# Performance work log

Measured on AMD Instinct MI355X. Metric: run time of the kernel, lower is better.

Reference implementation:

```python
import jax, jax.numpy as jnp
import numpy as np

N, M, A, F = 100000, 12, 64, 41  # atoms, neighbors, atom_fea_len, nbr_fea_len
EPS = 1e-5


def setup_inputs() -> dict:
    key = jax.random.key(0)
    ks = jax.random.split(key, 8)
    return {
        "atom_fea": jax.random.normal(ks[0], (N, A), jnp.float32),
        "nbr_fea": jax.random.normal(ks[1], (N, M, F), jnp.float32),
        "nbr_fea_idx": jax.random.randint(ks[2], (N, M), 0, N),
        "W_full": jax.random.normal(ks[3], (3, 2 * A + F, 2 * A), jnp.float32) / np.sqrt(2 * A + F).astype(np.float32),
        "b_full": jnp.zeros((3, 2 * A), jnp.float32),
        "g1": jnp.ones((3, 2 * A), jnp.float32),
        "bt1": jnp.zeros((3, 2 * A), jnp.float32),
        "g2": jnp.ones((3, A), jnp.float32),
        "bt2": jnp.zeros((3, A), jnp.float32),
        "W_scale": jax.random.normal(ks[4], (2, F, F), jnp.float32) / np.sqrt(F).astype(np.float32),
        "b_scale": jnp.zeros((2, F), jnp.float32),
        "W_fuse": jax.random.normal(ks[5], (3 * A, A), jnp.float32) / np.sqrt(3 * A).astype(np.float32),
        "b_fuse": jnp.zeros((A,), jnp.float32),
    }


def _bn(x, g, b):
    # training-mode BatchNorm1d over flattened leading dims (per-feature stats)
    x2 = x.reshape(-1, x.shape[-1])
    mu = x2.mean(0)
    var = x2.var(0)
    xn = (x2 - mu) * jax.lax.rsqrt(var + EPS)
    return (xn * g + b).reshape(x.shape)


def _conv_layer(atom_fea, nbr_fea, idx, W, b, g1, bt1, g2, bt2):
    # standard CGCNN ConvLayer
    nbr_atom = atom_fea[idx]                                   # [N,M,A] gather
    self_fea = jnp.broadcast_to(atom_fea[:, None, :], nbr_atom.shape)
    total = jnp.concatenate([self_fea, nbr_atom, nbr_fea], -1)  # [N,M,2A+F]
    z = _bn(total @ W + b, g1, bt1)                            # [N,M,2A]
    filt, core = jnp.split(z, 2, axis=-1)
    summed = (jax.nn.sigmoid(filt) * jax.nn.softplus(core)).sum(1)  # [N,A]
    summed = _bn(summed, g2, bt2)
    return jax.nn.softplus(atom_fea + summed)


def reference(atom_fea, nbr_fea, nbr_fea_idx, W_full, b_full, g1, bt1, g2, bt2,
              W_scale, b_scale, W_fuse, b_fuse):
    outs = []
    for i in range(3):  # scales [1, 2, 3]
        nf = nbr_fea if i == 0 else nbr_fea @ W_scale[i - 1] + b_scale[i - 1]
        outs.append(_conv_layer(atom_fea, nf, nbr_fea_idx,
                                W_full[i], b_full[i], g1[i], bt1[i], g2[i], bt2[i]))
    cat = jnp.concatenate(outs, -1)            # [N, 3A]
    return jax.nn.relu(cat @ W_fuse + b_fuse)  # [N, A]
```

## Files before the change

kernel.cpp:

```cpp
#include <hip/hip_runtime.h>
#include <math.h>

#define NATOMS 100000
#define M 12
#define A 64
#define F 41
#define C1 128
#define TOTF 169
#define NMROWS (NATOMS * M)

#define OFF_WEFF   0
#define OFF_BEFF   15744
#define OFF_SUM1   16128
#define OFF_SQ1    16512
#define OFF_SUM2   16896
#define OFF_SQ2    17088
#define OFF_SCA    17280
#define OFF_SHA    17664
#define OFF_SCB    18048
#define OFF_SHB    18240
#define OFF_P      32768
#define OFF_SUMMED (OFF_P + (size_t)NATOMS*768)
#define OFF_Q      OFF_P

__device__ __forceinline__ float sigmoidf_(float x) {
    return 1.0f / (1.0f + __expf(-x));
}
__device__ __forceinline__ float softplusf_(float x) {
    return fmaxf(x, 0.0f) + __logf(1.0f + __expf(-fabsf(x)));
}

__global__ void k_weff(const float* __restrict__ Wf, const float* __restrict__ bf,
                       const float* __restrict__ Wsc, const float* __restrict__ bsc,
                       float* __restrict__ ws) {
    int j = threadIdx.x;
    float* We = ws + OFF_WEFF;
    float* be = ws + OFF_BEFF;
    for (int s = 0; s < 3; ++s) {
        float bb = bf[s * C1 + j];
        if (s > 0) {
            for (int q = 0; q < F; ++q)
                bb += bsc[(s - 1) * F + q] * Wf[(s * TOTF + 128 + q) * C1 + j];
        }
        be[s * C1 + j] = bb;
        for (int k = 0; k < F; ++k) {
            float v;
            if (s == 0) {
                v = Wf[(0 * TOTF + 128 + k) * C1 + j];
            } else {
                v = 0.0f;
                for (int q = 0; q < F; ++q)
                    v += Wsc[((s - 1) * F + k) * F + q] * Wf[(s * TOTF + 128 + q) * C1 + j];
            }
            We[(s * F + k) * C1 + j] = v;
        }
    }
}

__global__ __launch_bounds__(256) void k_pall(const float* __restrict__ atom,
                                              const float* __restrict__ Wf,
                                              float* __restrict__ ws) {
    int u = threadIdx.x;
    int s = blockIdx.x;
    float wcol[A];
    int colw = u & 127;
#pragma unroll
    for (int k = 0; k < A; ++k) {
        int row = (u < 128) ? k : (A + k);
        wcol[k] = Wf[(s * TOTF + row) * C1 + colw];
    }
    float* P = ws + OFF_P;
    for (int a = blockIdx.y; a < NATOMS; a += gridDim.y) {
        const float* ar = atom + (size_t)a * A;
        float acc = 0.0f;
#pragma unroll
        for (int k = 0; k < A; ++k) acc = fmaf(ar[k], wcol[k], acc);
        P[(size_t)a * 768 + s * 256 + u] = acc;
    }
}

template <int PASS>
__global__ __launch_bounds__(192) void k_conv(const float* __restrict__ nbr,
                                              const int* __restrict__ idx,
                                              float* __restrict__ ws) {
    int tid = threadIdx.x;
    int s = tid >> 6;
    int j = tid & 63;
    const float* We = ws + OFF_WEFF;
    const float* be = ws + OFF_BEFF;
    const float* P = ws + OFF_P;
    float w1[F], w2[F];
#pragma unroll
    for (int k = 0; k < F; ++k) {
        w1[k] = We[(s * F + k) * C1 + j];
        w2[k] = We[(s * F + k) * C1 + 64 + j];
    }
    float b1 = be[s * C1 + j], b2 = be[s * C1 + 64 + j];
    float sc1 = 0.f, sh1 = 0.f, sc2 = 0.f, sh2 = 0.f;
    if (PASS == 1) {
        sc1 = ws[OFF_SCA + s * C1 + j];
        sh1 = ws[OFF_SHA + s * C1 + j];
        sc2 = ws[OFF_SCA + s * C1 + 64 + j];
        sh2 = ws[OFF_SHA + s * C1 + 64 + j];
    }
    float accA = 0.f, accB = 0.f, accC = 0.f, accD = 0.f;
    float* summed = ws + OFF_SUMMED;
    for (int a = blockIdx.x; a < NATOMS; a += gridDim.x) {
        float ps1 = P[(size_t)a * 768 + s * 256 + j];
        float ps2 = P[(size_t)a * 768 + s * 256 + 64 + j];
        float hsum = 0.0f;
        for (int m = 0; m < M; ++m) {
            int pair = a * M + m;
            int row = idx[pair];
            const float* x = nbr + (size_t)pair * F;
            float z1 = b1 + ps1 + P[(size_t)row * 768 + s * 256 + 128 + j];
            float z2 = b2 + ps2 + P[(size_t)row * 768 + s * 256 + 192 + j];
#pragma unroll
            for (int k = 0; k < F; ++k) {
                float xv = x[k];
                z1 = fmaf(xv, w1[k], z1);
                z2 = fmaf(xv, w2[k], z2);
            }
            if (PASS == 0) {
                accA += z1; accB += z1 * z1;
                accC += z2; accD += z2 * z2;
            } else {
                float f = fmaf(z1, sc1, sh1);
                float c = fmaf(z2, sc2, sh2);
                hsum += sigmoidf_(f) * softplusf_(c);
            }
        }
        if (PASS == 1) {
            summed[((size_t)s * NATOMS + a) * 64 + j] = hsum;
            accA += hsum;
            accB += hsum * hsum;
        }
    }
    if (PASS == 0) {
        atomicAdd(&ws[OFF_SUM1 + s * C1 + j], accA);
        atomicAdd(&ws[OFF_SQ1 + s * C1 + j], accB);
        atomicAdd(&ws[OFF_SUM1 + s * C1 + 64 + j], accC);
        atomicAdd(&ws[OFF_SQ1 + s * C1 + 64 + j], accD);
    } else {
        atomicAdd(&ws[OFF_SUM2 + s * 64 + j], accA);
        atomicAdd(&ws[OFF_SQ2 + s * 64 + j], accB);
    }
}

__global__ void k_bn1(const float* __restrict__ g1, const float* __restrict__ bt1,
                      float* __restrict__ ws) {
    int c = threadIdx.x;
    float inv = 1.0f / (float)NMROWS;
    float mu = ws[OFF_SUM1 + c] * inv;
    float var = ws[OFF_SQ1 + c] * inv - mu * mu;
    float rs = rsqrtf(var + 1e-5f);
    float g = g1[c];
    ws[OFF_SCA + c] = g * rs;
    ws[OFF_SHA + c] = bt1[c] - mu * rs * g;
}

__global__ void k_bn2(const float* __restrict__ g2, const float* __restrict__ bt2,
                      float* __restrict__ ws) {
    int c = threadIdx.x;
    float inv = 1.0f / (float)NATOMS;
    float mu = ws[OFF_SUM2 + c] * inv;
    float var = ws[OFF_SQ2 + c] * inv - mu * mu;
    float rs = rsqrtf(var + 1e-5f);
    float g = g2[c];
    ws[OFF_SCB + c] = g * rs;
    ws[OFF_SHB + c] = bt2[c] - mu * rs * g;
}

__global__ __launch_bounds__(256) void k_q(const float* __restrict__ atom,
                                           float* __restrict__ ws) {
    size_t e = (size_t)blockIdx.x * 256 + threadIdx.x;
    if (e >= (size_t)NATOMS * 192) return;
    int a = (int)(e / 192);
    int c = (int)(e % 192);
    int s = c >> 6;
    int j = c & 63;
    float v = ws[OFF_SUMMED + ((size_t)s * NATOMS + a) * 64 + j];
    v = fmaf(v, ws[OFF_SCB + c], ws[OFF_SHB + c]);
    v += atom[(size_t)a * A + j];
    ws[OFF_Q + (size_t)a * 192 + c] = softplusf_(v);
}

__global__ __launch_bounds__(64, 2) void k_fuse(const float* __restrict__ Wfu,
                                                const float* __restrict__ bfu,
                                                const float* __restrict__ ws,
                                                float* __restrict__ out) {
    int o = threadIdx.x;
    float wcol[192];
#pragma unroll
    for (int k = 0; k < 192; ++k) wcol[k] = Wfu[k * 64 + o];
    float bb = bfu[o];
    const float* q = ws + OFF_Q;
    for (int a = blockIdx.x; a < NATOMS; a += gridDim.x) {
        const float* qr = q + (size_t)a * 192;
        float acc = bb;
#pragma unroll
        for (int k = 0; k < 192; ++k) acc = fmaf(qr[k], wcol[k], acc);
        out[(size_t)a * 64 + o] = fmaxf(acc, 0.0f);
    }
}

extern "C" void kernel_launch(void* const* d_in, const int* in_sizes, int n_in,
                              void* d_out, int out_size, void* d_ws, size_t ws_size,
                              hipStream_t stream) {
    const float* atom = (const float*)d_in[0];
    const float* nbr  = (const float*)d_in[1];
    const int*   idx  = (const int*)d_in[2];
    const float* Wf   = (const float*)d_in[3];
    const float* bf   = (const float*)d_in[4];
    const float* g1   = (const float*)d_in[5];
    const float* bt1  = (const float*)d_in[6];
    const float* g2   = (const float*)d_in[7];
    const float* bt2  = (const float*)d_in[8];
    const float* Wsc  = (const float*)d_in[9];
    const float* bsc  = (const float*)d_in[10];
    const float* Wfu  = (const float*)d_in[11];
    const float* bfu  = (const float*)d_in[12];
    float* out = (float*)d_out;
    float* ws = (float*)d_ws;

    hipMemsetAsync((char*)d_ws + OFF_SUM1 * sizeof(float), 0, 1152 * sizeof(float), stream);

    k_weff<<<1, 128, 0, stream>>>(Wf, bf, Wsc, bsc, ws);
    k_pall<<<dim3(3, 512), 256, 0, stream>>>(atom, Wf, ws);
    k_conv<0><<<1280, 192, 0, stream>>>(nbr, idx, ws);
    k_bn1<<<1, 384, 0, stream>>>(g1, bt1, ws);
    k_conv<1><<<1280, 192, 0, stream>>>(nbr, idx, ws);
    k_bn2<<<1, 192, 0, stream>>>(g2, bt2, ws);
    k_q<<<(NATOMS * 192 + 255) / 256, 256, 0, stream>>>(atom, ws);
    k_fuse<<<2048, 64, 0, stream>>>(Wfu, bfu, ws, out);
}
```

Baseline: 2.648 ms.

## Vectorize weight loads, interleave P columns, split fuse reduction across two waves

Effective neighbor weights are stored per output column, padded to 44 floats, so k_conv can load them as float4. The k_pall output is interleaved so filter and core values come out as a single float2 per atom and per gathered neighbor. Atom rows in k_pall are read as float4, and occupancy hints are added through launch_bounds. k_fuse splits the 192-long dot product across two wavefronts, handles 8 atoms per iteration and combines the halves through double-buffered shared memory. The aim is fewer scalar loads and less register pressure, at the cost of a changed workspace layout and an added barrier in k_fuse.

```diff
diff --git a/kernel.cpp b/kernel.cpp
--- a/kernel.cpp
+++ b/kernel.cpp
@@ -5,23 +5,24 @@
 #define M 12
 #define A 64
 #define F 41
+#define FP 44
 #define C1 128
 #define TOTF 169
 #define NMROWS (NATOMS * M)
 
-#define OFF_WEFF   0
-#define OFF_BEFF   15744
-#define OFF_SUM1   16128
-#define OFF_SQ1    16512
-#define OFF_SUM2   16896
-#define OFF_SQ2    17088
-#define OFF_SCA    17280
-#define OFF_SHA    17664
-#define OFF_SCB    18048
-#define OFF_SHB    18240
-#define OFF_P      32768
+#define OFF_WEFF 0
+#define OFF_BEFF 16896
+#define OFF_SUM1 17280
+#define OFF_SQ1  17664
+#define OFF_SUM2 18048
+#define OFF_SQ2  18240
+#define OFF_SCA  18432
+#define OFF_SHA  18816
+#define OFF_SCB  19200
+#define OFF_SHB  19392
+#define OFF_P    32768
 #define OFF_SUMMED (OFF_P + (size_t)NATOMS*768)
-#define OFF_Q      OFF_P
+#define OFF_Q    OFF_P
 
 __device__ __forceinline__ float sigmoidf_(float x) {
     return 1.0f / (1.0f + __expf(-x));
@@ -43,6 +44,7 @@
                 bb += bsc[(s - 1) * F + q] * Wf[(s * TOTF + 128 + q) * C1 + j];
         }
         be[s * C1 + j] = bb;
+        float* dst = We + (size_t)(s * 128 + j) * FP;
         for (int k = 0; k < F; ++k) {
             float v;
             if (s == 0) {
@@ -52,50 +54,61 @@
                 for (int q = 0; q < F; ++q)
                     v += Wsc[((s - 1) * F + k) * F + q] * Wf[(s * TOTF + 128 + q) * C1 + j];
             }
-            We[(s * F + k) * C1 + j] = v;
-        }
-    }
-}
-
-__global__ __launch_bounds__(256) void k_pall(const float* __restrict__ atom,
-                                              const float* __restrict__ Wf,
-                                              float* __restrict__ ws) {
+            dst[k] = v;
+        }
+        for (int k = F; k < FP; ++k) dst[k] = 0.0f;
+    }
+}
+
+__global__ __launch_bounds__(256, 4) void k_pall(const float* __restrict__ atom,
+                                                 const float* __restrict__ Wf,
+                                                 float* __restrict__ ws) {
     int u = threadIdx.x;
     int s = blockIdx.x;
+    int v = u & 127;
+    int part = u >> 7;
+    int j = v >> 1;
+    int role = v & 1;
+    int col = role * 64 + j;
+    int rowbase = part * 64;
     float wcol[A];
-    int colw = u & 127;
-#pragma unroll
-    for (int k = 0; k < A; ++k) {
-        int row = (u < 128) ? k : (A + k);
-        wcol[k] = Wf[(s * TOTF + row) * C1 + colw];
-    }
+#pragma unroll
+    for (int k = 0; k < A; ++k)
+        wcol[k] = Wf[(s * TOTF + rowbase + k) * C1 + col];
     float* P = ws + OFF_P;
+#pragma unroll 1
     for (int a = blockIdx.y; a < NATOMS; a += gridDim.y) {
-        const float* ar = atom + (size_t)a * A;
+        const float4* ar4 = (const float4*)(atom + (size_t)a * A);
         float acc = 0.0f;
 #pragma unroll
-        for (int k = 0; k < A; ++k) acc = fmaf(ar[k], wcol[k], acc);
+        for (int t = 0; t < 16; ++t) {
+            float4 av = ar4[t];
+            acc = fmaf(av.x, wcol[4 * t + 0], acc);
+            acc = fmaf(av.y, wcol[4 * t + 1], acc);
+            acc = fmaf(av.z, wcol[4 * t + 2], acc);
+            acc = fmaf(av.w, wcol[4 * t + 3], acc);
+        }
         P[(size_t)a * 768 + s * 256 + u] = acc;
     }
 }
 
 template <int PASS>
-__global__ __launch_bounds__(192) void k_conv(const float* __restrict__ nbr,
-                                              const int* __restrict__ idx,
-                                              float* __restrict__ ws) {
+__global__ __launch_bounds__(192, 4) void k_conv(const float* __restrict__ nbr,
+                                                 const int* __restrict__ idx,
+                                                 float* __restrict__ ws) {
     int tid = threadIdx.x;
     int s = tid >> 6;
     int j = tid & 63;
-    const float* We = ws + OFF_WEFF;
-    const float* be = ws + OFF_BEFF;
     const float* P = ws + OFF_P;
-    float w1[F], w2[F];
-#pragma unroll
-    for (int k = 0; k < F; ++k) {
-        w1[k] = We[(s * F + k) * C1 + j];
-        w2[k] = We[(s * F + k) * C1 + 64 + j];
-    }
-    float b1 = be[s * C1 + j], b2 = be[s * C1 + 64 + j];
+
+    const float4* wt1 = (const float4*)(ws + OFF_WEFF + (size_t)(s * 128 + j) * FP);
+    const float4* wt2 = (const float4*)(ws + OFF_WEFF + (size_t)(s * 128 + 64 + j) * FP);
+    float4 w1v[11], w2v[11];
+#pragma unroll
+    for (int t = 0; t < 11; ++t) { w1v[t] = wt1[t]; w2v[t] = wt2[t]; }
+
+    float b1 = ws[OFF_BEFF + s * C1 + j];
+    float b2 = ws[OFF_BEFF + s * C1 + 64 + j];
     float sc1 = 0.f, sh1 = 0.f, sc2 = 0.f, sh2 = 0.f;
     if (PASS == 1) {
         sc1 = ws[OFF_SCA + s * C1 + j];
@@ -105,35 +118,47 @@
     }
     float accA = 0.f, accB = 0.f, accC = 0.f, accD = 0.f;
     float* summed = ws + OFF_SUMMED;
+
+#pragma unroll 1
     for (int a = blockIdx.x; a < NATOMS; a += gridDim.x) {
-        float ps1 = P[(size_t)a * 768 + s * 256 + j];
-        float ps2 = P[(size_t)a * 768 + s * 256 + 64 + j];
+        const float2 ps = *(const float2*)(P + (size_t)a * 768 + s * 256 + 2 * j);
         float hsum = 0.0f;
+#pragma unroll 1
         for (int m = 0; m < M; ++m) {
             int pair = a * M + m;
             int row = idx[pair];
             const float* x = nbr + (size_t)pair * F;
-            float z1 = b1 + ps1 + P[(size_t)row * 768 + s * 256 + 128 + j];
-            float z2 = b2 + ps2 + P[(size_t)row * 768 + s * 256 + 192 + j];
-#pragma unroll
-            for (int k = 0; k < F; ++k) {
-                float xv = x[k];
-                z1 = fmaf(xv, w1[k], z1);
-                z2 = fmaf(xv, w2[k], z2);
-            }
+            const float2 gn = *(const float2*)(P + (size_t)row * 768 + s * 256 + 128 + 2 * j);
+            float z1 = b1 + ps.x + gn.x;
+            float z2 = b2 + ps.y + gn.y;
+#pragma unroll
+            for (int t = 0; t < 10; ++t) {
+                float x0 = x[4 * t + 0], x1 = x[4 * t + 1], x2 = x[4 * t + 2], x3 = x[4 * t + 3];
+                z1 = fmaf(x0, w1v[t].x, z1);
+                z2 = fmaf(x0, w2v[t].x, z2);
+                z1 = fmaf(x1, w1v[t].y, z1);
+                z2 = fmaf(x1, w2v[t].y, z2);
+                z1 = fmaf(x2, w1v[t].z, z1);
+                z2 = fmaf(x2, w2v[t].z, z2);
+                z1 = fmaf(x3, w1v[t].w, z1);
+                z2 = fmaf(x3, w2v[t].w, z2);
+            }
+            float x40 = x[40];
+            z1 = fmaf(x40, w1v[10].x, z1);
+            z2 = fmaf(x40, w2v[10].x, z2);
             if (PASS == 0) {
-                accA += z1; accB += z1 * z1;
-                accC += z2; accD += z2 * z2;
+                accA += z1; accB = fmaf(z1, z1, accB);
+                accC += z2; accD = fmaf(z2, z2, accD);
             } else {
                 float f = fmaf(z1, sc1, sh1);
                 float c = fmaf(z2, sc2, sh2);
-                hsum += sigmoidf_(f) * softplusf_(c);
+                hsum = fmaf(sigmoidf_(f), softplusf_(c), hsum);
             }
         }
         if (PASS == 1) {
             summed[((size_t)s * NATOMS + a) * 64 + j] = hsum;
             accA += hsum;
-            accB += hsum * hsum;
+            accB = fmaf(hsum, hsum, accB);
         }
     }
     if (PASS == 0) {
@@ -185,22 +210,53 @@
     ws[OFF_Q + (size_t)a * 192 + c] = softplusf_(v);
 }
 
-__global__ __launch_bounds__(64, 2) void k_fuse(const float* __restrict__ Wfu,
-                                                const float* __restrict__ bfu,
-                                                const float* __restrict__ ws,
-                                                float* __restrict__ out) {
-    int o = threadIdx.x;
-    float wcol[192];
-#pragma unroll
-    for (int k = 0; k < 192; ++k) wcol[k] = Wfu[k * 64 + o];
+__global__ __launch_bounds__(128, 3) void k_fuse(const float* __restrict__ Wfu,
+                                                 const float* __restrict__ bfu,
+                                                 const float* __restrict__ ws,
+                                                 float* __restrict__ out) {
+    int w = threadIdx.x >> 6;
+    int o = threadIdx.x & 63;
+    __shared__ float sp[2][8][64];
+    float4 wv[24];
+#pragma unroll
+    for (int t = 0; t < 24; ++t) {
+        int k = w * 96 + 4 * t;
+        wv[t].x = Wfu[(k + 0) * 64 + o];
+        wv[t].y = Wfu[(k + 1) * 64 + o];
+        wv[t].z = Wfu[(k + 2) * 64 + o];
+        wv[t].w = Wfu[(k + 3) * 64 + o];
+    }
     float bb = bfu[o];
     const float* q = ws + OFF_Q;
-    for (int a = blockIdx.x; a < NATOMS; a += gridDim.x) {
-        const float* qr = q + (size_t)a * 192;
-        float acc = bb;
-#pragma unroll
-        for (int k = 0; k < 192; ++k) acc = fmaf(qr[k], wcol[k], acc);
-        out[(size_t)a * 64 + o] = fmaxf(acc, 0.0f);
+    int p = 0;
+#pragma unroll 1
+    for (int cid = blockIdx.x; cid < NATOMS / 8; cid += gridDim.x) {
+        float acc[8];
+#pragma unroll
+        for (int i = 0; i < 8; ++i) {
+            const float4* q4 = (const float4*)(q + (size_t)(cid * 8 + i) * 192 + w * 96);
+            float a0 = 0.f, a1 = 0.f, a2 = 0.f, a3 = 0.f;
+#pragma unroll
+            for (int t = 0; t < 24; ++t) {
+                float4 xq = q4[t];
+                a0 = fmaf(xq.x, wv[t].x, a0);
+                a1 = fmaf(xq.y, wv[t].y, a1);
+                a2 = fmaf(xq.z, wv[t].z, a2);
+                a3 = fmaf(xq.w, wv[t].w, a3);
+            }
+            acc[i] = (a0 + a1) + (a2 + a3);
+        }
+        if (w == 1) {
+#pragma unroll
+            for (int i = 0; i < 8; ++i) sp[p][i][o] = acc[i];
+        }
+        __syncthreads();
+        if (w == 0) {
+#pragma unroll
+            for (int i = 0; i < 8; ++i)
+                out[(size_t)(cid * 8 + i) * 64 + o] = fmaxf(acc[i] + sp[p][i][o] + bb, 0.0f);
+        }
+        p ^= 1;
     }
 }
 
@@ -232,5 +288,5 @@
     k_conv<1><<<1280, 192, 0, stream>>>(nbr, idx, ws);
     k_bn2<<<1, 192, 0, stream>>>(g2, bt2, ws);
     k_q<<<(NATOMS * 192 + 255) / 256, 256, 0, stream>>>(atom, ws);
-    k_fuse<<<2048, 64, 0, stream>>>(Wfu, bfu, ws, out);
-}
+    k_fuse<<<2048, 128, 0, stream>>>(Wfu, bfu, ws, out);
+}
```

After: 2.680 ms. No clear change (+1.2%).
